# Optimization experiments

Hardware: AMD Instinct MI355X
Metric: run time of the kernel (lower is better)

The kernel has to match this reference:

```python
import jax, jax.numpy as jnp
import numpy as np

N, E = 50000, 800000
DIN, DH, DOUT = 128, 128, 64


def _w(k, fan_in, fan_out):
    return (jax.random.normal(k, (fan_in, fan_out), jnp.float32) / np.sqrt(fan_in)).astype(jnp.float32)


def setup_inputs() -> dict:
    key = jax.random.key(0)
    ks = jax.random.split(key, 12)
    x = jax.random.normal(ks[0], (N, DIN), jnp.float32)
    edge_index = jax.random.randint(ks[1], (2, E), 0, N, dtype=jnp.int64)
    return {
        "x": x,
        "edge_index": edge_index,
        # sage1 block: SAGEConv(DIN->DH) -> relu -> SAGEConv(DH->DH)
        "Ws11": _w(ks[2], DIN, DH), "Wn11": _w(ks[3], DIN, DH), "b11": jnp.zeros((DH,), jnp.float32),
        "Ws12": _w(ks[4], DH, DH),  "Wn12": _w(ks[5], DH, DH),  "b12": jnp.zeros((DH,), jnp.float32),
        # sage2 block: SAGEConv(DH->DH) -> relu -> SAGEConv(DH->DH)
        "Ws21": _w(ks[6], DH, DH),  "Wn21": _w(ks[7], DH, DH),  "b21": jnp.zeros((DH,), jnp.float32),
        "Ws22": _w(ks[8], DH, DH),  "Wn22": _w(ks[9], DH, DH),  "b22": jnp.zeros((DH,), jnp.float32),
        # classifier
        "Wc": _w(ks[10], DH, DOUT), "bc": jnp.zeros((DOUT,), jnp.float32),
    }


def _sage_conv(h, src, tgt, Ws, Wn, b, n):
    # mean-aggregate neighbor features (src -> tgt), then self + neighbor linear
    msgs = h[src]                                                   # [E, d] gather
    deg = jax.ops.segment_sum(jnp.ones((src.shape[0],), h.dtype), tgt, num_segments=n)
    agg = jax.ops.segment_sum(msgs, tgt, num_segments=n)
    agg = agg / jnp.maximum(deg, 1.0)[:, None]                      # [n, d]
    return h @ Ws + agg @ Wn + b


def reference(x, edge_index, Ws11, Wn11, b11, Ws12, Wn12, b12,
              Ws21, Wn21, b21, Ws22, Wn22, b22, Wc, bc):
    src, tgt = edge_index[0], edge_index[1]
    n = x.shape[0]
    # sage1 block (2 layers) + outer relu
    h = jax.nn.relu(_sage_conv(x, src, tgt, Ws11, Wn11, b11, n))
    h = _sage_conv(h, src, tgt, Ws12, Wn12, b12, n)
    h = jax.nn.relu(h)
    # dropout (eval mode): identity
    # sage2 block (2 layers) + outer relu
    h = jax.nn.relu(_sage_conv(h, src, tgt, Ws21, Wn21, b21, n))
    h = _sage_conv(h, src, tgt, Ws22, Wn22, b22, n)
    h = jax.nn.relu(h)
    # global mean pool over nodes, then classify
    g = jnp.mean(h, axis=0)                                         # [DH]
    return g @ Wc + bc                                              # [DOUT]
```

## Files before the change

### kernel.cpp

```cpp
#include <hip/hip_runtime.h>
#include <hip/hip_bf16.h>
#include <hip/hip_fp16.h>


typedef _Float16 f16x8 __attribute__((ext_vector_type(8)));
typedef _Float16 f16x4 __attribute__((ext_vector_type(4)));
typedef float f32x4 __attribute__((ext_vector_type(4)));

__global__ void k_deg(const int* __restrict__ tgt, int* __restrict__ deg, int E) {
  int e = blockIdx.x * blockDim.x + threadIdx.x;
  if (e < E) atomicAdd(&deg[tgt[e]], 1);
}

__global__ __launch_bounds__(256) void k_scan1(const int* __restrict__ deg,
                                               int* __restrict__ partial,
                                               int* __restrict__ blocksum,
                                               float* __restrict__ inv_deg, int n) {
  __shared__ int s[256];
  int tid = threadIdx.x;
  int i = blockIdx.x * 256 + tid;
  int v = (i < n) ? deg[i] : 0;
  s[tid] = v;
  __syncthreads();
  for (int off = 1; off < 256; off <<= 1) {
    int t = (tid >= off) ? s[tid - off] : 0;
    __syncthreads();
    s[tid] += t;
    __syncthreads();
  }
  if (i < n) {
    partial[i] = s[tid] - v;
    inv_deg[i] = 1.0f / fmaxf((float)v, 1.0f);
  }
  if (tid == 255) blocksum[blockIdx.x] = s[255];
}

__global__ __launch_bounds__(256) void k_scan2(int* __restrict__ blocksum, int nb) {
  __shared__ int s[256];
  int tid = threadIdx.x;
  int v = (tid < nb) ? blocksum[tid] : 0;
  s[tid] = v;
  __syncthreads();
  for (int off = 1; off < 256; off <<= 1) {
    int t = (tid >= off) ? s[tid - off] : 0;
    __syncthreads();
    s[tid] += t;
    __syncthreads();
  }
  if (tid < nb) blocksum[tid] = s[tid] - v;
}

__global__ __launch_bounds__(256) void k_scan3(const int* __restrict__ partial,
                                               const int* __restrict__ blocksum,
                                               int* __restrict__ row_start,
                                               int* __restrict__ cursor, int n, int E) {
  int i = blockIdx.x * 256 + threadIdx.x;
  if (i < n) {
    int r = partial[i] + blocksum[blockIdx.x];
    row_start[i] = r;
    cursor[i] = r;
  }
  if (i == 0) row_start[n] = E;
}

__global__ void k_scatter(const int* __restrict__ src, const int* __restrict__ tgt,
                          int* __restrict__ cursor, int* __restrict__ csr_src, int E) {
  int e = blockIdx.x * blockDim.x + threadIdx.x;
  if (e < E) {
    int t = tgt[e];
    int pos = atomicAdd(&cursor[t], 1);
    csr_src[pos] = src[e];
  }
}

__global__ __launch_bounds__(256) void k_cvt_x(const float* __restrict__ x,
                                               __half* __restrict__ xh, int total8) {
  int i = blockIdx.x * 256 + threadIdx.x;
  if (i >= total8) return;
  const float4* p = (const float4*)(x + (size_t)i * 8);
  float4 v0 = p[0], v1 = p[1];
  f16x8 o;
  o[0] = (_Float16)v0.x; o[1] = (_Float16)v0.y; o[2] = (_Float16)v0.z; o[3] = (_Float16)v0.w;
  o[4] = (_Float16)v1.x; o[5] = (_Float16)v1.y; o[6] = (_Float16)v1.z; o[7] = (_Float16)v1.w;
  *(f16x8*)(xh + (size_t)i * 8) = o;
}

struct WPack {
  const float* s[4];
  const float* n[4];
};

__global__ __launch_bounds__(256) void k_prep_w(WPack p, __half* __restrict__ Wt) {
  int l = blockIdx.y;
  int i = blockIdx.x * 256 + threadIdx.x;
  int n = i >> 8;
  int k = i & 255;
  const float* W = (k < 128) ? p.s[l] : p.n[l];
  float v = W[(size_t)(k & 127) * 128 + n];
  Wt[(size_t)l * 32768 + (size_t)n * 256 + k] = __float2half(v);
}

__global__ __launch_bounds__(256) void k_agg_h(
    const __half* __restrict__ h, const int* __restrict__ csr_src,
    const int* __restrict__ row_start, const float* __restrict__ inv_deg,
    __half* __restrict__ agg, int n_nodes) {
  int gw = (blockIdx.x * 256 + (int)threadIdx.x) >> 6;
  int lane = threadIdx.x & 63;
  if (gw >= n_nodes) return;
  int q = lane >> 4;
  int dl = (lane & 15) * 8;
  int beg = row_start[gw];
  int end = row_start[gw + 1];
  float a0 = 0.f, a1 = 0.f, a2 = 0.f, a3 = 0.f;
  float a4 = 0.f, a5 = 0.f, a6 = 0.f, a7 = 0.f;
  int e = beg;
  for (; e + 16 <= end; e += 16) {
    int i0 = csr_src[e + q];
    int i1 = csr_src[e + 4 + q];
    int i2 = csr_src[e + 8 + q];
    int i3 = csr_src[e + 12 + q];
    f16x8 v0 = *(const f16x8*)(h + (size_t)i0 * 128 + dl);
    f16x8 v1 = *(const f16x8*)(h + (size_t)i1 * 128 + dl);
    f16x8 v2 = *(const f16x8*)(h + (size_t)i2 * 128 + dl);
    f16x8 v3 = *(const f16x8*)(h + (size_t)i3 * 128 + dl);
    a0 += ((float)v0[0] + (float)v1[0]) + ((float)v2[0] + (float)v3[0]);
    a1 += ((float)v0[1] + (float)v1[1]) + ((float)v2[1] + (float)v3[1]);
    a2 += ((float)v0[2] + (float)v1[2]) + ((float)v2[2] + (float)v3[2]);
    a3 += ((float)v0[3] + (float)v1[3]) + ((float)v2[3] + (float)v3[3]);
    a4 += ((float)v0[4] + (float)v1[4]) + ((float)v2[4] + (float)v3[4]);
    a5 += ((float)v0[5] + (float)v1[5]) + ((float)v2[5] + (float)v3[5]);
    a6 += ((float)v0[6] + (float)v1[6]) + ((float)v2[6] + (float)v3[6]);
    a7 += ((float)v0[7] + (float)v1[7]) + ((float)v2[7] + (float)v3[7]);
  }
  for (; e + 8 <= end; e += 8) {
    int i0 = csr_src[e + q];
    int i1 = csr_src[e + 4 + q];
    f16x8 v0 = *(const f16x8*)(h + (size_t)i0 * 128 + dl);
    f16x8 v1 = *(const f16x8*)(h + (size_t)i1 * 128 + dl);
    a0 += (float)v0[0] + (float)v1[0];
    a1 += (float)v0[1] + (float)v1[1];
    a2 += (float)v0[2] + (float)v1[2];
    a3 += (float)v0[3] + (float)v1[3];
    a4 += (float)v0[4] + (float)v1[4];
    a5 += (float)v0[5] + (float)v1[5];
    a6 += (float)v0[6] + (float)v1[6];
    a7 += (float)v0[7] + (float)v1[7];
  }
  for (; e + 4 <= end; e += 4) {
    int i0 = csr_src[e + q];
    f16x8 v0 = *(const f16x8*)(h + (size_t)i0 * 128 + dl);
    a0 += (float)v0[0];
    a1 += (float)v0[1];
    a2 += (float)v0[2];
    a3 += (float)v0[3];
    a4 += (float)v0[4];
    a5 += (float)v0[5];
    a6 += (float)v0[6];
    a7 += (float)v0[7];
  }
  if (e + q < end) {
    int i0 = csr_src[e + q];
    f16x8 v0 = *(const f16x8*)(h + (size_t)i0 * 128 + dl);
    a0 += (float)v0[0];
    a1 += (float)v0[1];
    a2 += (float)v0[2];
    a3 += (float)v0[3];
    a4 += (float)v0[4];
    a5 += (float)v0[5];
    a6 += (float)v0[6];
    a7 += (float)v0[7];
  }
  a0 += __shfl_xor(a0, 16, 64);
  a1 += __shfl_xor(a1, 16, 64);
  a2 += __shfl_xor(a2, 16, 64);
  a3 += __shfl_xor(a3, 16, 64);
  a4 += __shfl_xor(a4, 16, 64);
  a5 += __shfl_xor(a5, 16, 64);
  a6 += __shfl_xor(a6, 16, 64);
  a7 += __shfl_xor(a7, 16, 64);
  a0 += __shfl_xor(a0, 32, 64);
  a1 += __shfl_xor(a1, 32, 64);
  a2 += __shfl_xor(a2, 32, 64);
  a3 += __shfl_xor(a3, 32, 64);
  a4 += __shfl_xor(a4, 32, 64);
  a5 += __shfl_xor(a5, 32, 64);
  a6 += __shfl_xor(a6, 32, 64);
  a7 += __shfl_xor(a7, 32, 64);
  if (q == 0) {
    float wgt = inv_deg[gw];
    f16x8 r;
    r[0] = (_Float16)(a0 * wgt);
    r[1] = (_Float16)(a1 * wgt);
    r[2] = (_Float16)(a2 * wgt);
    r[3] = (_Float16)(a3 * wgt);
    r[4] = (_Float16)(a4 * wgt);
    r[5] = (_Float16)(a5 * wgt);
    r[6] = (_Float16)(a6 * wgt);
    r[7] = (_Float16)(a7 * wgt);
    *(f16x8*)(agg + (size_t)gw * 128 + dl) = r;
  }
}

__global__ __launch_bounds__(256) void k_linear_mfma(
    const __half* __restrict__ h, const __half* __restrict__ agg,
    const __half* __restrict__ Wt, const float* __restrict__ bias,
    __half* __restrict__ out, int n_nodes) {
  int tid = threadIdx.x;
  int wave = tid >> 6;
  int lane = tid & 63;
  int m0 = blockIdx.x * 64 + wave * 16;
  int lr = lane & 15;
  int lg = lane >> 4;
  f32x4 acc[8];
#pragma unroll
  for (int ct = 0; ct < 8; ++ct) acc[ct] = (f32x4){0.f, 0.f, 0.f, 0.f};

  int arow = m0 + lr;
  if (arow >= n_nodes) arow = n_nodes - 1;
  const __half* hrow = h + (size_t)arow * 128;
  const __half* grow = agg + (size_t)arow * 128;

#pragma unroll
  for (int ks = 0; ks < 8; ++ks) {
    const __half* srcp = (ks < 4) ? hrow : grow;
    int koff = (ks & 3) * 32 + lg * 8;
    f16x8 a = *(const f16x8*)(srcp + koff);
    int kb = ks * 32 + lg * 8;
#pragma unroll
    for (int ct = 0; ct < 8; ++ct) {
      f16x8 b = *(const f16x8*)(Wt + (size_t)(ct * 16 + lr) * 256 + kb);
      acc[ct] = __builtin_amdgcn_mfma_f32_16x16x32_f16(a, b, acc[ct], 0, 0, 0);
    }
  }

#pragma unroll
  for (int ct = 0; ct < 8; ++ct) {
    int n_col = ct * 16 + lr;
    float bv = bias[n_col];
#pragma unroll
    for (int r = 0; r < 4; ++r) {
      int m = m0 + lg * 4 + r;
      if (m < n_nodes)
        out[(size_t)m * 128 + n_col] = __float2half(fmaxf(acc[ct][r] + bv, 0.f));
    }
  }
}

__global__ __launch_bounds__(256) void k_pool(const __half* __restrict__ h,
                                              float* __restrict__ partial, int n_nodes) {
  __shared__ float red[4][128];
  int tid = threadIdx.x;
  int lane = tid & 63;
  int w = tid >> 6;
  float a0 = 0.f, a1 = 0.f;
  for (int n = blockIdx.x * 4 + w; n < n_nodes; n += gridDim.x * 4) {
    float2 f = __half22float2(*(const __half2*)(h + (size_t)n * 128 + lane * 2));
    a0 += f.x;
    a1 += f.y;
  }
  red[w][lane * 2] = a0;
  red[w][lane * 2 + 1] = a1;
  __syncthreads();
  if (tid < 128) {
    partial[(size_t)blockIdx.x * 128 + tid] =
        (red[0][tid] + red[1][tid]) + (red[2][tid] + red[3][tid]);
  }
}

__global__ __launch_bounds__(512) void k_final(const float* __restrict__ partial,
                                               const float* __restrict__ Wc,
                                               const float* __restrict__ bc,
                                               float* __restrict__ out, int n_nodes) {
  __shared__ float red[4][128];
  __shared__ float gs[128];
  __shared__ float red2[8][64];
  int tid = threadIdx.x;
  int j = tid & 127;
  int c = tid >> 7;
  float s = 0.f;
#pragma unroll
  for (int b = 0; b < 64; ++b) s += partial[(size_t)(c * 64 + b) * 128 + j];
  red[c][j] = s;
  __syncthreads();
  if (tid < 128) {
    float g = (red[0][tid] + red[1][tid]) + (red[2][tid] + red[3][tid]);
    gs[tid] = g / (float)n_nodes;
  }
  __syncthreads();
  {
    int jo = tid & 63;
    int c2 = tid >> 6;
    float s2 = 0.f;
#pragma unroll
    for (int d = 0; d < 16; ++d)
      s2 += gs[c2 * 16 + d] * Wc[(size_t)(c2 * 16 + d) * 64 + jo];
    red2[c2][jo] = s2;
  }
  __syncthreads();
  if (tid < 64) {
    float o = bc[tid];
#pragma unroll
    for (int c2 = 0; c2 < 8; ++c2) o += red2[c2][tid];
    out[tid] = o;
  }
}

extern "C" void kernel_launch(void* const* d_in, const int* in_sizes, int n_in,
                              void* d_out, int out_size, void* d_ws, size_t ws_size,
                              hipStream_t stream) {
  const float* x = (const float*)d_in[0];
  const int* ei = (const int*)d_in[1];
  const float* Ws11 = (const float*)d_in[2];
  const float* Wn11 = (const float*)d_in[3];
  const float* b11 = (const float*)d_in[4];
  const float* Ws12 = (const float*)d_in[5];
  const float* Wn12 = (const float*)d_in[6];
  const float* b12 = (const float*)d_in[7];
  const float* Ws21 = (const float*)d_in[8];
  const float* Wn21 = (const float*)d_in[9];
  const float* b21 = (const float*)d_in[10];
  const float* Ws22 = (const float*)d_in[11];
  const float* Wn22 = (const float*)d_in[12];
  const float* b22 = (const float*)d_in[13];
  const float* Wc = (const float*)d_in[14];
  const float* bc = (const float*)d_in[15];

  int N = in_sizes[0] / 128;
  int E = in_sizes[1] / 2;
  const int* src = ei;
  const int* tgt = ei + E;

  char* w = (char*)d_ws;
  size_t off = 0;
  auto alloc = [&](size_t bytes) {
    void* p = w + off;
    off += (bytes + 255) & ~(size_t)255;
    return p;
  };
  __half* xh = (__half*)alloc((size_t)N * 128 * 2);
  __half* hA = (__half*)alloc((size_t)N * 128 * 2);
  __half* hB = (__half*)alloc((size_t)N * 128 * 2);
  __half* aggb = (__half*)alloc((size_t)N * 128 * 2);
  __half* Wt = (__half*)alloc((size_t)4 * 32768 * 2);
  float* partial = (float*)alloc((size_t)256 * 128 * 4);
  float* inv_deg = (float*)alloc((size_t)N * 4);
  int* deg = (int*)alloc((size_t)N * 4);
  int* row_start = (int*)alloc((size_t)(N + 1) * 4);
  int* cursor = (int*)alloc((size_t)N * 4);
  int* csr_src = (int*)alloc((size_t)E * 4);
  int* scanp = (int*)alloc((size_t)N * 4);
  int* blocksum = (int*)alloc((size_t)256 * 4);

  hipMemsetAsync(deg, 0, (size_t)N * 4, stream);
  hipMemsetAsync(partial, 0, (size_t)256 * 128 * 4, stream);
  int eb = (E + 255) / 256;
  int nb = (N + 255) / 256;
  k_deg<<<eb, 256, 0, stream>>>(tgt, deg, E);
  k_scan1<<<nb, 256, 0, stream>>>(deg, scanp, blocksum, inv_deg, N);
  k_scan2<<<1, 256, 0, stream>>>(blocksum, nb);
  k_scan3<<<nb, 256, 0, stream>>>(scanp, blocksum, row_start, cursor, N, E);
  k_scatter<<<eb, 256, 0, stream>>>(src, tgt, cursor, csr_src, E);

  int total8 = N * 128 / 8;
  k_cvt_x<<<(total8 + 255) / 256, 256, 0, stream>>>(x, xh, total8);
  WPack wp;
  wp.s[0] = Ws11; wp.s[1] = Ws12; wp.s[2] = Ws21; wp.s[3] = Ws22;
  wp.n[0] = Wn11; wp.n[1] = Wn12; wp.n[2] = Wn21; wp.n[3] = Wn22;
  k_prep_w<<<dim3(128, 4), 256, 0, stream>>>(wp, Wt);

  int ab = (N + 3) / 4;
  int lb = (N + 63) / 64;

  k_agg_h<<<ab, 256, 0, stream>>>(xh, csr_src, row_start, inv_deg, aggb, N);
  k_linear_mfma<<<lb, 256, 0, stream>>>(xh, aggb, Wt + 0 * 32768, b11, hA, N);
  k_agg_h<<<ab, 256, 0, stream>>>(hA, csr_src, row_start, inv_deg, aggb, N);
  k_linear_mfma<<<lb, 256, 0, stream>>>(hA, aggb, Wt + 1 * 32768, b12, hB, N);
  k_agg_h<<<ab, 256, 0, stream>>>(hB, csr_src, row_start, inv_deg, aggb, N);
  k_linear_mfma<<<lb, 256, 0, stream>>>(hB, aggb, Wt + 2 * 32768, b21, hA, N);
  k_agg_h<<<ab, 256, 0, stream>>>(hA, csr_src, row_start, inv_deg, aggb, N);
  k_linear_mfma<<<lb, 256, 0, stream>>>(hA, aggb, Wt + 3 * 32768, b22, hB, N);

  k_pool<<<256, 256, 0, stream>>>(hB, partial, N);
  k_final<<<1, 512, 0, stream>>>(partial, Wc, bc, (float*)d_out, N);
}
```

Baseline: 399.8 us.

## Bucket edges by target range before CSR scatter to localize atomics

Replaces the degree-count and scatter kernels with a two-pass bucketing scheme. The first kernel counts degrees and partitions (tgt,src) pairs into 8 target-range buckets through shared-memory staging. The second kernel scatters each bucket into CSR, so cursor atomics and csr_src writes land in a narrower address range, which should improve cache locality. In exchange it adds an extra round trip through global memory for the 8-byte pairs, and a bucket could overflow its fixed capacity if the edges are skewed.

```diff
diff --git a/kernel.cpp b/kernel.cpp
--- a/kernel.cpp
+++ b/kernel.cpp
@@ -4,12 +4,74 @@
 
 
 typedef _Float16 f16x8 __attribute__((ext_vector_type(8)));
-typedef _Float16 f16x4 __attribute__((ext_vector_type(4)));
 typedef float f32x4 __attribute__((ext_vector_type(4)));
 
-__global__ void k_deg(const int* __restrict__ tgt, int* __restrict__ deg, int E) {
-  int e = blockIdx.x * blockDim.x + threadIdx.x;
-  if (e < E) atomicAdd(&deg[tgt[e]], 1);
+__global__ __launch_bounds__(256) void k_bucket(
+    const int* __restrict__ src, const int* __restrict__ tgt,
+    int* __restrict__ deg, unsigned long long* __restrict__ staging,
+    int* __restrict__ bucket_fill, int E, int bdiv, int cap) {
+  __shared__ unsigned long long buf[8][512];
+  __shared__ int cnt[8];
+  __shared__ int base[8];
+  int tid = threadIdx.x;
+  if (tid < 8) cnt[tid] = 0;
+  __syncthreads();
+  int e0 = blockIdx.x * 2048;
+#pragma unroll
+  for (int i = 0; i < 8; ++i) {
+    int e = e0 + i * 256 + tid;
+    if (e < E) {
+      int t = tgt[e];
+      int s = src[e];
+      atomicAdd(&deg[t], 1);
+      int b = t / bdiv;
+      unsigned long long pair =
+          ((unsigned long long)(unsigned)t << 32) | (unsigned)s;
+      int p = atomicAdd(&cnt[b], 1);
+      if (p < 512) {
+        buf[b][p] = pair;
+      } else {
+        int gp = atomicAdd(&bucket_fill[b], 1);
+        staging[(size_t)b * cap + gp] = pair;
+      }
+    }
+  }
+  __syncthreads();
+  if (tid < 8) {
+    int c = min(cnt[tid], 512);
+    base[tid] = atomicAdd(&bucket_fill[tid], c);
+    cnt[tid] = c;
+  }
+  __syncthreads();
+  for (int b = 0; b < 8; ++b) {
+    int c = cnt[b];
+    for (int p = tid; p < c; p += 256)
+      staging[(size_t)b * cap + base[b] + p] = buf[b][p];
+  }
+}
+
+__global__ __launch_bounds__(256) void k_scatter2(
+    const unsigned long long* __restrict__ staging,
+    const int* __restrict__ bucket_fill, int* __restrict__ cursor,
+    int* __restrict__ csr_src, int cap) {
+  int b = blockIdx.x & 7;
+  int nchunk = gridDim.x >> 3;
+  int chunk = blockIdx.x >> 3;
+  int n = bucket_fill[b];
+  const unsigned long long* sb = staging + (size_t)b * cap;
+  for (int i0 = chunk * 2048; i0 < n; i0 += nchunk * 2048) {
+#pragma unroll
+    for (int t = 0; t < 8; ++t) {
+      int i = i0 + t * 256 + (int)threadIdx.x;
+      if (i < n) {
+        unsigned long long pair = sb[i];
+        int tg = (int)(pair >> 32);
+        int s = (int)(pair & 0xffffffffu);
+        int pos = atomicAdd(&cursor[tg], 1);
+        csr_src[pos] = s;
+      }
+    }
+  }
 }
 
 __global__ __launch_bounds__(256) void k_scan1(const int* __restrict__ deg,
@@ -61,16 +123,6 @@
     cursor[i] = r;
   }
   if (i == 0) row_start[n] = E;
-}
-
-__global__ void k_scatter(const int* __restrict__ src, const int* __restrict__ tgt,
-                          int* __restrict__ cursor, int* __restrict__ csr_src, int E) {
-  int e = blockIdx.x * blockDim.x + threadIdx.x;
-  if (e < E) {
-    int t = tgt[e];
-    int pos = atomicAdd(&cursor[t], 1);
-    csr_src[pos] = src[e];
-  }
 }
 
 __global__ __launch_bounds__(256) void k_cvt_x(const float* __restrict__ x,
@@ -330,6 +382,9 @@
   const int* src = ei;
   const int* tgt = ei + E;
 
+  int bdiv = (N + 7) / 8;
+  int cap = E / 8 + 8192;
+
   char* w = (char*)d_ws;
   size_t off = 0;
   auto alloc = [&](size_t bytes) {
@@ -350,16 +405,21 @@
   int* csr_src = (int*)alloc((size_t)E * 4);
   int* scanp = (int*)alloc((size_t)N * 4);
   int* blocksum = (int*)alloc((size_t)256 * 4);
+  unsigned long long* staging =
+      (unsigned long long*)alloc((size_t)8 * cap * 8);
+  int* bucket_fill = (int*)alloc((size_t)8 * 4);
 
   hipMemsetAsync(deg, 0, (size_t)N * 4, stream);
+  hipMemsetAsync(bucket_fill, 0, 8 * 4, stream);
   hipMemsetAsync(partial, 0, (size_t)256 * 128 * 4, stream);
-  int eb = (E + 255) / 256;
+
   int nb = (N + 255) / 256;
-  k_deg<<<eb, 256, 0, stream>>>(tgt, deg, E);
+  int bb = (E + 2047) / 2048;
+  k_bucket<<<bb, 256, 0, stream>>>(src, tgt, deg, staging, bucket_fill, E, bdiv, cap);
   k_scan1<<<nb, 256, 0, stream>>>(deg, scanp, blocksum, inv_deg, N);
   k_scan2<<<1, 256, 0, stream>>>(blocksum, nb);
   k_scan3<<<nb, 256, 0, stream>>>(scanp, blocksum, row_start, cursor, N, E);
-  k_scatter<<<eb, 256, 0, stream>>>(src, tgt, cursor, csr_src, E);
+  k_scatter2<<<448, 256, 0, stream>>>(staging, bucket_fill, cursor, csr_src, cap);
 
   int total8 = N * 128 / 8;
   k_cvt_x<<<(total8 + 255) / 256, 256, 0, stream>>>(x, xh, total8);
```

After: 389.2 us. -2.6%, faster.
